# Kernel optimization log

Hardware: AMD Instinct MI355X
Metric: run time of the kernel (lower is better)

The kernel has to match this reference:

```python
import jax, jax.numpy as jnp
import numpy as np
from jax import lax
from jax.scipy.special import logsumexp

C, H, W = 21, 512, 512
ITERS = 5
THETA_GAMMA = 3.0
THETA_ALPHA = 160.0
MAX_RADIUS = 8  # truncation cap for the Gaussian surrogate of the permutohedral filter
# deterministic stand-in for random.sample(range(200,400),1) per iteration
SP_IDS = [250 + 7 * i for i in range(ITERS)]


def _gauss_kernel(sigma):
    radius = min(int(2.0 * sigma + 0.5), MAX_RADIUS)
    t = np.arange(-radius, radius + 1, dtype=np.float32)
    k = np.exp(-0.5 * (t / np.float32(sigma)) ** 2)
    k /= k.sum()
    return jnp.asarray(k)


def _blur(x, k):
    # x: (c,h,w); separable Gaussian blur as surrogate for custom high_dim_filter
    x4 = x[:, None]                      # (c,1,h,w), c acts as batch
    kh = k.reshape(1, 1, -1, 1)
    kw = k.reshape(1, 1, 1, -1)
    y = lax.conv_general_dilated(x4, kh, (1, 1), 'SAME')
    y = lax.conv_general_dilated(y, kw, (1, 1), 'SAME')
    return y[:, 0]


def _sp_containment_update(q, low_w, high_w, sp_map, sp_idx):
    # q: softmax output (c,h,w); sp_map: (h,w) int ids; single clique sp_idx
    cond = (sp_map == sp_idx)                       # (h,w)
    condf = cond.astype(q.dtype)[None]              # (1,h,w) broadcast over c
    q_clique = condf * q                            # masked q
    bool_max = (q == q.max(axis=0, keepdims=True))  # global per-pixel argmax mask
    maxlab = q_clique.max(axis=0, keepdims=True)    # per-pixel max label prob in clique
    l_eq = (bool_max & cond[None]).astype(q.dtype) * q
    A_np = q_clique + maxlab - l_eq                 # "A no padding"
    q_sum = A_np                                    # sum over the single clique
    # per-class logsumexp over the whole plane (zeros outside clique, as in source)
    B_sp = logsumexp(q_clique, axis=(1, 2))         # (c,)
    prod_sp = condf * B_sp[:, None, None]
    B_cont = logsumexp(A_np, axis=(1, 2))           # (c,)
    prod_io = condf * B_cont[:, None, None]         # cond applied twice in source == once
    q_mod = q + (q == 0).astype(q.dtype)
    q_sum = q_sum + (q_sum == 0).astype(q.dtype)
    ft = prod_sp / q_mod
    sp_update = low_w[0][:, None, None] * ft + high_w[0] * (1.0 - ft)
    ft2 = prod_io / q_sum
    cont_update = low_w[1][:, None, None] * ft2 + high_w[1] * (1.0 - ft2)
    return sp_update + cont_update


def setup_inputs() -> dict:
    key = jax.random.key(0)
    k1, k2, k3 = jax.random.split(key, 3)
    unaries = jax.random.normal(k1, (1, H, W, C), dtype=jnp.float32)
    rgb = jax.random.uniform(k2, (1, H, W, 3), dtype=jnp.float32)
    sp_map = jax.random.randint(k3, (1, W, H), 0, 400, dtype=jnp.int32)
    spatial_ker_weights = jnp.eye(C, dtype=jnp.float32)
    bilateral_ker_weights = jnp.eye(C, dtype=jnp.float32)
    complex_rel_low_weights = jnp.ones((2, C), dtype=jnp.float32)
    complex_rel_high_weights = jnp.ones((2,), dtype=jnp.float32)
    compatibility_matrix = -jnp.eye(C, dtype=jnp.float32)
    return {
        'unaries': unaries, 'rgb': rgb, 'sp_map': sp_map,
        'spatial_ker_weights': spatial_ker_weights,
        'bilateral_ker_weights': bilateral_ker_weights,
        'complex_rel_low_weights': complex_rel_low_weights,
        'complex_rel_high_weights': complex_rel_high_weights,
        'compatibility_matrix': compatibility_matrix,
    }


def reference(unaries, rgb, sp_map, spatial_ker_weights, bilateral_ker_weights,
              complex_rel_low_weights, complex_rel_high_weights, compatibility_matrix):
    u = jnp.transpose(unaries[0], (2, 0, 1))   # (c,h,w)
    sp = jnp.transpose(sp_map[0])              # (h,w)
    k_sp = _gauss_kernel(THETA_GAMMA)
    k_bi = _gauss_kernel(THETA_ALPHA)
    ones = jnp.ones((C, H, W), jnp.float32)
    spatial_norm = _blur(ones, k_sp)
    bilateral_norm = _blur(ones, k_bi)
    q = u
    for i in range(ITERS):
        sm = jax.nn.softmax(q, axis=0)
        spatial_out = _blur(sm, k_sp) / spatial_norm
        bilateral_out = _blur(sm, k_bi) / bilateral_norm
        cont = _sp_containment_update(sm, complex_rel_low_weights,
                                      complex_rel_high_weights, sp, SP_IDS[i])
        mp = (jnp.einsum('ij,jhw->ihw', spatial_ker_weights, spatial_out)
              + jnp.einsum('ij,jhw->ihw', bilateral_ker_weights, bilateral_out))
        pairwise = jnp.einsum('ij,jhw->ihw', compatibility_matrix, mp)
        q = u - pairwise - cont
    return jnp.transpose(q, (1, 2, 0))[None]   # (1,h,w,c)
```

## Files before the change

### kernel.cpp

```cpp
#include <hip/hip_runtime.h>
#include <hip/hip_bf16.h>
#include <math.h>
#include <utility>

#define C 21
#define H 512
#define W 512
#define HW (H*W)
#define CHW (C*HW)
#define N_ITERS 5
#define RSP 6
#define KSP 13
#define RBI 8
#define KBI 17
#define LIST_CAP 4096

#define KSP_OFF   0
#define KBI_OFF   16
#define NSP_OFF   64
#define NBI_OFF   576
#define M1_OFF    1088
#define M2_OFF    1536
#define NCOND_OFF 2048
#define S1_OFF    2064
#define S2_OFF    2176
#define CTR_OFF   2288
#define LIST_OFF  2304
#define CONTB_OFF 22784
#define UBH_OFF   131072
#define QB16_OFF  (UBH_OFF + CHW/2)
#define T12_OFF   (QB16_OFF + CHW/2)

#define REP21(F) F(0) F(1) F(2) F(3) F(4) F(5) F(6) F(7) F(8) F(9) F(10) \
                 F(11) F(12) F(13) F(14) F(15) F(16) F(17) F(18) F(19) F(20)

template <int... Js, typename F>
__device__ __forceinline__ void sfor(std::integer_sequence<int, Js...>, F&& f) {
  (f(std::integral_constant<int, Js>{}), ...);
}
#define SFOR(N, ...) sfor(std::make_integer_sequence<int, N>{}, __VA_ARGS__)

__device__ __forceinline__ float bf2f(unsigned short u) {
  return __uint_as_float(((unsigned)u) << 16);
}
__device__ __forceinline__ unsigned short f2bfu(float a) {
  __hip_bfloat16 h = __float2bfloat16(a);
  return *(unsigned short*)&h;
}
__device__ __forceinline__ unsigned packbf(float a, float b) {
  return (unsigned)f2bfu(a) | ((unsigned)f2bfu(b) << 16);
}

__global__ __launch_bounds__(512) void k_setup(float* ws, const float* skw,
                                               const float* bkw, const float* cm) {
  int tid = threadIdx.x;
  if (tid == 0) {
    float s = 0.f;
    for (int i = 0; i < KSP; ++i) {
      float t = (float)(i - RSP);
      float v = expf(-0.5f * (t / 3.0f) * (t / 3.0f));
      ws[KSP_OFF + i] = v; s += v;
    }
    for (int i = 0; i < KSP; ++i) ws[KSP_OFF + i] /= s;
    s = 0.f;
    for (int i = 0; i < KBI; ++i) {
      float t = (float)(i - RBI);
      float v = expf(-0.5f * (t / 160.0f) * (t / 160.0f));
      ws[KBI_OFF + i] = v; s += v;
    }
    for (int i = 0; i < KBI; ++i) ws[KBI_OFF + i] /= s;
  }
  __syncthreads();
  if (tid < H) {
    float nsp = 0.f, nbi = 0.f;
    for (int t = 0; t < KSP; ++t) { int x = tid + t - RSP; if (x >= 0 && x < H) nsp += ws[KSP_OFF + t]; }
    for (int t = 0; t < KBI; ++t) { int x = tid + t - RBI; if (x >= 0 && x < H) nbi += ws[KBI_OFF + t]; }
    ws[NSP_OFF + tid] = 1.f / nsp;
    ws[NBI_OFF + tid] = 1.f / nbi;
  }
  if (tid < C * C) {
    int i = tid / C, j = tid % C;
    float m1 = 0.f, m2 = 0.f;
    for (int k = 0; k < C; ++k) {
      m1 += cm[i * C + k] * skw[k * C + j];
      m2 += cm[i * C + k] * bkw[k * C + j];
    }
    ws[M1_OFF + tid] = m1;
    ws[M2_OFF + tid] = m2;
  }
  if (tid < N_ITERS * C) { ws[S1_OFF + tid] = 0.f; ws[S2_OFF + tid] = 0.f; }
  if (tid < N_ITERS) {
    ((int*)(ws + NCOND_OFF))[tid] = 0;
    ((int*)(ws + CTR_OFF))[tid] = 0;
  }
}

__global__ __launch_bounds__(256) void k_spt_tin(const int* __restrict__ sp_map,
                                                 const float* __restrict__ in,
                                                 int* __restrict__ ncond,
                                                 int* __restrict__ list,
                                                 unsigned* __restrict__ ubh32,
                                                 unsigned* __restrict__ qb32) {
  __shared__ float t[C * 257];
  int tid = threadIdx.x;
  int p = blockIdx.x * 256 + tid;
  {
    int h = p >> 9, w = p & 511;
    int v = sp_map[w * H + h];
#pragma unroll
    for (int i = 0; i < N_ITERS; ++i)
      if (v == 250 + 7 * i) {
        int slot = atomicAdd(&ncond[i], 1);
        if (slot < LIST_CAP) list[i * LIST_CAP + slot] = p;
      }
  }
  size_t p0 = (size_t)blockIdx.x * 256;
  size_t fbase = p0 * C;
#pragma unroll
  for (int i = 0; i < C; ++i) {
    int e = i * 256 + tid;
    int pp = e / C, c = e % C;
    t[c * 257 + pp] = in[fbase + e];
  }
  __syncthreads();
  if (tid < 128) {
#pragma unroll
    for (int c = 0; c < C; ++c) {
      float v0 = t[c * 257 + 2 * tid];
      float v1 = t[c * 257 + 2 * tid + 1];
      unsigned d = packbf(v0, v1);
      size_t di = ((size_t)c * HW + p0) / 2 + tid;
      ubh32[di] = d;
      qb32[di] = d;
    }
  }
}

__global__ __launch_bounds__(256) void k_tout(const unsigned* __restrict__ qb32,
                                              float* __restrict__ out) {
  __shared__ float t[C * 257];
  int tid = threadIdx.x;
  size_t p0 = (size_t)blockIdx.x * 256;
  if (tid < 128) {
#pragma unroll
    for (int c = 0; c < C; ++c) {
      unsigned d = qb32[((size_t)c * HW + p0) / 2 + tid];
      t[c * 257 + 2 * tid] = __uint_as_float(d << 16);
      t[c * 257 + 2 * tid + 1] = __uint_as_float(d & 0xFFFF0000u);
    }
  }
  __syncthreads();
  size_t fbase = p0 * C;
#pragma unroll
  for (int i = 0; i < C; ++i) {
    int e = i * 256 + tid;
    int p = e / C, c = e % C;
    out[fbase + e] = t[c * 257 + p];
  }
}

__global__ __launch_bounds__(256) void k_clique(const unsigned short* __restrict__ qh,
                                                float* __restrict__ ws,
                                                const float* __restrict__ loww,
                                                const float* __restrict__ highw,
                                                int iter) {
  int tid = threadIdx.x;
  const int* ncond = (const int*)(ws + NCOND_OFF);
  const int* list = (const int*)(ws + LIST_OFF) + iter * LIST_CAP;
  int n = ncond[iter]; if (n > LIST_CAP) n = LIST_CAP;
#define D1(i) float s1_##i = 0.f, s2_##i = 0.f;
  REP21(D1)
#undef D1
  for (int j = blockIdx.x * 256 + tid; j < n; j += 1024) {
    int p = list[j];
#define LQ(i) float q##i = __expf(bf2f(qh[(size_t)(i) * HW + p]));
    REP21(LQ)
#undef LQ
    float s = ((((q0+q1)+(q2+q3))+((q4+q5)+(q6+q7)))+(((q8+q9)+(q10+q11))+((q12+q13)+(q14+q15))))+(((q16+q17)+(q18+q19))+q20);
    float inv = 1.f / s;
    float smax = 0.f;
#define NM(i) q##i *= inv; smax = fmaxf(smax, q##i);
    REP21(NM)
#undef NM
#define AC(i) { s1_##i += __expf(q##i); \
                float A = (q##i == smax) ? smax : q##i + smax; \
                s2_##i += __expf(A); }
    REP21(AC)
#undef AC
  }
#define RED(x) x += __shfl_xor(x, 32); x += __shfl_xor(x, 16); x += __shfl_xor(x, 8); \
               x += __shfl_xor(x, 4); x += __shfl_xor(x, 2); x += __shfl_xor(x, 1);
#define RD(i) RED(s1_##i) RED(s2_##i)
  REP21(RD)
#undef RD
#undef RED
  if ((tid & 63) == 0) {
#define AT(i) atomicAdd(&ws[S1_OFF + iter * C + (i)], s1_##i); \
              atomicAdd(&ws[S2_OFF + iter * C + (i)], s2_##i);
    REP21(AT)
#undef AT
  }
  __threadfence();
  __syncthreads();
  if (tid == 0) {
    int* ctr = (int*)(ws + CTR_OFF) + iter;
    atomicAdd(ctr, 1);
    while (atomicAdd(ctr, 0) < 4) { __builtin_amdgcn_s_sleep(1); }
  }
  __syncthreads();
  __threadfence();
  float HWn = (float)(HW - n);
#define LB(i) float lb1_##i = logf(HWn + ws[S1_OFF + iter * C + (i)]); \
              float lb2_##i = logf(HWn + ws[S2_OFF + iter * C + (i)]);
  REP21(LB)
#undef LB
  float high0 = highw[0], high1 = highw[1];
  float* contb = ws + CONTB_OFF;
  for (int j = blockIdx.x * 256 + tid; j < n; j += 1024) {
    int p = list[j];
#define LQ2(i) float q##i = __expf(bf2f(qh[(size_t)(i) * HW + p]));
    REP21(LQ2)
#undef LQ2
    float s = ((((q0+q1)+(q2+q3))+((q4+q5)+(q6+q7)))+(((q8+q9)+(q10+q11))+((q12+q13)+(q14+q15))))+(((q16+q17)+(q18+q19))+q20);
    float inv = 1.f / s;
    float smax = 0.f;
#define NM2(i) q##i *= inv; smax = fmaxf(smax, q##i);
    REP21(NM2)
#undef NM2
#define CW(i) { float A = (q##i == smax) ? smax : q##i + smax; \
                float ft = lb1_##i / q##i; \
                float ft2 = lb2_##i / A; \
                contb[j * C + (i)] = loww[i] * ft + high0 * (1.f - ft) \
                                   + loww[C + (i)] * ft2 + high1 * (1.f - ft2); }
    REP21(CW)
#undef CW
  }
}

__global__ __launch_bounds__(256) void k_smmix(const unsigned* __restrict__ q16x2,
                                               unsigned* __restrict__ t12,
                                               const float* __restrict__ ws) {
  int tid = threadIdx.x;
  int b2 = blockIdx.x * 256 + tid;
#define LQ(i) unsigned d##i = q16x2[(size_t)(i) * (HW/2) + b2]; \
              float ex##i = __expf(__uint_as_float(d##i << 16)); \
              float ey##i = __expf(__uint_as_float(d##i & 0xFFFF0000u));
  REP21(LQ)
#undef LQ
  float sa = ((((ex0+ex1)+(ex2+ex3))+((ex4+ex5)+(ex6+ex7)))+(((ex8+ex9)+(ex10+ex11))+((ex12+ex13)+(ex14+ex15))))+(((ex16+ex17)+(ex18+ex19))+ex20);
  float sb = ((((ey0+ey1)+(ey2+ey3))+((ey4+ey5)+(ey6+ey7)))+(((ey8+ey9)+(ey10+ey11))+((ey12+ey13)+(ey14+ey15))))+(((ey16+ey17)+(ey18+ey19))+ey20);
  float ia = 1.f / sa, ib = 1.f / sb;
#define NQ(i) ex##i *= ia; ey##i *= ib;
  REP21(NQ)
#undef NQ
  for (int i = 0; i < C; ++i) {
    const float* r1 = ws + M1_OFF + i * C;
    const float* r2 = ws + M2_OFF + i * C;
    float t1a = 0.f, t1b = 0.f, t2a = 0.f, t2b = 0.f;
#define MIX(c) { float m1v = r1[c], m2v = r2[c]; \
                 t1a += m1v * ex##c; t1b += m1v * ey##c; \
                 t2a += m2v * ex##c; t2b += m2v * ey##c; }
    REP21(MIX)
#undef MIX
    uint2 st;
    st.x = packbf(t1a, t2a);
    st.y = packbf(t1b, t2b);
    *reinterpret_cast<uint2*>(t12 + (size_t)i * HW + 2 * b2) = st;
  }
}

__global__ __launch_bounds__(256) void k_blur2d(
    const unsigned* __restrict__ t12, const unsigned* __restrict__ uh32,
    unsigned* __restrict__ qout, const float* __restrict__ ws,
    const float* __restrict__ highw) {
  __shared__ float asmem[16 * 152], bsmem[16 * 152];
  __shared__ float ktsp[KSP], ktbi[KBI];
  __shared__ float nspw[128], nbiw[128], nsph[16], nbih[16];
  int tid = threadIdx.x;
  int l = blockIdx.x;
  int nl = (l & 7) * 336 + (l >> 3);
  int c = nl >> 7;
  int rem = nl & 127;
  int h0 = (rem >> 2) * 16;
  int w0 = (rem & 3) * 128;
  if (tid < KSP) ktsp[tid] = ws[KSP_OFF + tid];
  if (tid >= 32 && tid < 32 + KBI) ktbi[tid - 32] = ws[KBI_OFF + tid - 32];
  if (tid >= 64 && tid < 192) {
    int i = tid - 64;
    nspw[i] = ws[NSP_OFF + w0 + i];
    nbiw[i] = ws[NBI_OFF + w0 + i];
  }
  if (tid >= 192 && tid < 208) {
    int i = tid - 192;
    nsph[i] = ws[NSP_OFF + h0 + i];
    nbih[i] = ws[NBI_OFF + h0 + i];
  }
  __syncthreads();
  size_t cbase = (size_t)c * HW;
  if (tid < 144) {
    int col = w0 - 8 + tid;
    bool okc = (col >= 0 && col < W);
    const unsigned* s12 = t12 + cbase;
    unsigned lv[32];
    SFOR(32, [&](auto jc) {
      constexpr int j = decltype(jc)::value;
      int hh = h0 - 8 + j;
      lv[j] = (okc && hh >= 0 && hh < H) ? s12[(size_t)hh * W + col] : 0u;
    });
    float a[16], b[16];
    SFOR(16, [&](auto oc) {
      constexpr int o = decltype(oc)::value;
      a[o] = 0.f; b[o] = 0.f;
    });
    SFOR(32, [&](auto jc) {
      constexpr int j = decltype(jc)::value;
      float f1 = __uint_as_float(lv[j] << 16);
      float f2 = __uint_as_float(lv[j] & 0xFFFF0000u);
      SFOR(16, [&](auto oc) {
        constexpr int o = decltype(oc)::value;
        if constexpr (j - 2 - o >= 0 && j - 2 - o < KSP) a[o] += ktsp[j - 2 - o] * f1;
        if constexpr (j - o >= 0 && j - o < KBI) b[o] += ktbi[j - o] * f2;
      });
    });
    SFOR(16, [&](auto oc) {
      constexpr int o = decltype(oc)::value;
      asmem[o * 152 + tid] = a[o];
      bsmem[o * 152 + tid] = b[o];
    });
  }
  __syncthreads();
  float cc = highw[0] + highw[1];
#pragma unroll
  for (int k = 0; k < 2; ++k) {
    int o = tid + k * 256;
    int r = o >> 5;
    int wq = (o & 31) * 4;
    float aw[16], bw[20];
    const float2* ap = reinterpret_cast<const float2*>(&asmem[r * 152 + wq + 2]);
    const float2* bp = reinterpret_cast<const float2*>(&bsmem[r * 152 + wq]);
    SFOR(8, [&](auto jc) {
      constexpr int j = decltype(jc)::value;
      float2 v = ap[j];
      aw[2 * j] = v.x;
      aw[2 * j + 1] = v.y;
    });
    SFOR(10, [&](auto jc) {
      constexpr int j = decltype(jc)::value;
      float2 v = bp[j];
      bw[2 * j] = v.x;
      bw[2 * j + 1] = v.y;
    });
    float ao[4], bo[4];
    SFOR(4, [&](auto jc) {
      constexpr int j = decltype(jc)::value;
      float s1 = 0.f;
      float s2 = 0.f;
      SFOR(KSP, [&](auto tc) {
        constexpr int t = decltype(tc)::value;
        s1 += ktsp[t] * aw[j + t];
      });
      SFOR(KBI, [&](auto tc) {
        constexpr int t = decltype(tc)::value;
        s2 += ktbi[t] * bw[j + t];
      });
      ao[j] = s1;
      bo[j] = s2;
    });
    int hh = h0 + r, ww = w0 + wq;
    size_t idx = cbase + (size_t)hh * W + ww;
    uint2 uv = *reinterpret_cast<const uint2*>(uh32 + (idx >> 1));
    float u0 = __uint_as_float(uv.x << 16);
    float u1 = __uint_as_float(uv.x & 0xFFFF0000u);
    float u2 = __uint_as_float(uv.y << 16);
    float u3 = __uint_as_float(uv.y & 0xFFFF0000u);
    float nh1 = nsph[r], nh2 = nbih[r];
    float r0 = u0 - (ao[0] * (nh1 * nspw[wq])     + bo[0] * (nh2 * nbiw[wq]))     - cc;
    float r1 = u1 - (ao[1] * (nh1 * nspw[wq + 1]) + bo[1] * (nh2 * nbiw[wq + 1])) - cc;
    float r2 = u2 - (ao[2] * (nh1 * nspw[wq + 2]) + bo[2] * (nh2 * nbiw[wq + 2])) - cc;
    float r3 = u3 - (ao[3] * (nh1 * nspw[wq + 3]) + bo[3] * (nh2 * nbiw[wq + 3])) - cc;
    uint2 st;
    st.x = packbf(r0, r1);
    st.y = packbf(r2, r3);
    *reinterpret_cast<uint2*>(qout + (idx >> 1)) = st;
  }
}

__global__ __launch_bounds__(256) void k_contfix(unsigned short* __restrict__ q16,
                                                 const float* __restrict__ ws,
                                                 const float* __restrict__ highw,
                                                 int iter) {
  const int* ncond = (const int*)(ws + NCOND_OFF);
  int n = ncond[iter]; if (n > LIST_CAP) n = LIST_CAP;
  int e = blockIdx.x * 256 + threadIdx.x;
  if (e >= n * C) return;
  int j = e / C, c = e - j * C;
  const int* list = (const int*)(ws + LIST_OFF) + iter * LIST_CAP;
  int p = list[j];
  float cc = highw[0] + highw[1];
  float delta = cc - ws[CONTB_OFF + e];
  size_t idx = (size_t)c * HW + p;
  q16[idx] = f2bfu(bf2f(q16[idx]) + delta);
}

extern "C" void kernel_launch(void* const* d_in, const int* in_sizes, int n_in,
                              void* d_out, int out_size, void* d_ws, size_t ws_size,
                              hipStream_t stream) {
  const float* unaries = (const float*)d_in[0];
  const int* sp_map = (const int*)d_in[2];
  const float* skw = (const float*)d_in[3];
  const float* bkw = (const float*)d_in[4];
  const float* loww = (const float*)d_in[5];
  const float* highw = (const float*)d_in[6];
  const float* cm = (const float*)d_in[7];
  float* out = (float*)d_out;
  float* ws = (float*)d_ws;
  unsigned* ubh32 = (unsigned*)(ws + UBH_OFF);
  unsigned* qb32 = (unsigned*)(ws + QB16_OFF);
  unsigned short* qh16 = (unsigned short*)(ws + QB16_OFF);
  unsigned* t12 = (unsigned*)(ws + T12_OFF);
  int* ncond = (int*)(ws + NCOND_OFF);
  int* list = (int*)(ws + LIST_OFF);

  k_setup<<<1, 512, 0, stream>>>(ws, skw, bkw, cm);
  k_spt_tin<<<HW / 256, 256, 0, stream>>>(sp_map, unaries, ncond, list, ubh32, qb32);
  for (int i = 0; i < N_ITERS; ++i) {
    k_clique<<<4, 256, 0, stream>>>(qh16, ws, loww, highw, i);
    k_smmix<<<HW / 512, 256, 0, stream>>>(qb32, t12, ws);
    k_blur2d<<<2688, 256, 0, stream>>>(t12, ubh32, qb32, ws, highw);
    k_contfix<<<128, 256, 0, stream>>>(qh16, ws, highw, i);
  }
  k_tout<<<HW / 256, 256, 0, stream>>>(qb32, out);
}
```

Before: 373.2 us.

## Fuse contfix into next clique, drop duplicate q copy, coalesce sp_map reads

Result: slower. 415.6 us (+11.4%).

```diff
diff --git a/kernel.cpp b/kernel.cpp
--- a/kernel.cpp
+++ b/kernel.cpp
@@ -99,14 +99,13 @@
                                                  const float* __restrict__ in,
                                                  int* __restrict__ ncond,
                                                  int* __restrict__ list,
-                                                 unsigned* __restrict__ ubh32,
-                                                 unsigned* __restrict__ qb32) {
+                                                 unsigned* __restrict__ ubh32) {
   __shared__ float t[C * 257];
   int tid = threadIdx.x;
-  int p = blockIdx.x * 256 + tid;
   {
-    int h = p >> 9, w = p & 511;
-    int v = sp_map[w * H + h];
+    int m = blockIdx.x * 256 + tid;
+    int v = sp_map[m];
+    int p = ((m & 511) << 9) | (m >> 9);
 #pragma unroll
     for (int i = 0; i < N_ITERS; ++i)
       if (v == 250 + 7 * i) {
@@ -123,16 +122,11 @@
     t[c * 257 + pp] = in[fbase + e];
   }
   __syncthreads();
-  if (tid < 128) {
-#pragma unroll
-    for (int c = 0; c < C; ++c) {
-      float v0 = t[c * 257 + 2 * tid];
-      float v1 = t[c * 257 + 2 * tid + 1];
-      unsigned d = packbf(v0, v1);
-      size_t di = ((size_t)c * HW + p0) / 2 + tid;
-      ubh32[di] = d;
-      qb32[di] = d;
-    }
+  for (int e = tid; e < C * 128; e += 256) {
+    int c = e >> 7, pr = e & 127;
+    float v0 = t[c * 257 + 2 * pr];
+    float v1 = t[c * 257 + 2 * pr + 1];
+    ubh32[((size_t)c * HW + p0) / 2 + pr] = packbf(v0, v1);
   }
 }
 
@@ -159,7 +153,7 @@
   }
 }
 
-__global__ __launch_bounds__(256) void k_clique(const unsigned short* __restrict__ qh,
+__global__ __launch_bounds__(256) void k_clique(unsigned short* __restrict__ qh,
                                                 float* __restrict__ ws,
                                                 const float* __restrict__ loww,
                                                 const float* __restrict__ highw,
@@ -168,6 +162,18 @@
   const int* ncond = (const int*)(ws + NCOND_OFF);
   const int* list = (const int*)(ws + LIST_OFF) + iter * LIST_CAP;
   int n = ncond[iter]; if (n > LIST_CAP) n = LIST_CAP;
+  float high0 = highw[0], high1 = highw[1];
+  float cc = high0 + high1;
+  if (iter > 0) {
+    int np = ncond[iter - 1]; if (np > LIST_CAP) np = LIST_CAP;
+    const int* plist = (const int*)(ws + LIST_OFF) + (iter - 1) * LIST_CAP;
+    for (int e = blockIdx.x * 256 + tid; e < np * C; e += 1024) {
+      int j = e / C, c = e - j * C;
+      int p = plist[j];
+      size_t idx = (size_t)c * HW + p;
+      qh[idx] = f2bfu(bf2f(qh[idx]) + cc - ws[CONTB_OFF + e]);
+    }
+  }
 #define D1(i) float s1_##i = 0.f, s2_##i = 0.f;
   REP21(D1)
 #undef D1
@@ -214,7 +220,6 @@
               float lb2_##i = logf(HWn + ws[S2_OFF + iter * C + (i)]);
   REP21(LB)
 #undef LB
-  float high0 = highw[0], high1 = highw[1];
   float* contb = ws + CONTB_OFF;
   for (int j = blockIdx.x * 256 + tid; j < n; j += 1024) {
     int p = list[j];
@@ -417,17 +422,20 @@
   unsigned* ubh32 = (unsigned*)(ws + UBH_OFF);
   unsigned* qb32 = (unsigned*)(ws + QB16_OFF);
   unsigned short* qh16 = (unsigned short*)(ws + QB16_OFF);
+  unsigned short* uh16 = (unsigned short*)(ws + UBH_OFF);
   unsigned* t12 = (unsigned*)(ws + T12_OFF);
   int* ncond = (int*)(ws + NCOND_OFF);
   int* list = (int*)(ws + LIST_OFF);
 
   k_setup<<<1, 512, 0, stream>>>(ws, skw, bkw, cm);
-  k_spt_tin<<<HW / 256, 256, 0, stream>>>(sp_map, unaries, ncond, list, ubh32, qb32);
+  k_spt_tin<<<HW / 256, 256, 0, stream>>>(sp_map, unaries, ncond, list, ubh32);
   for (int i = 0; i < N_ITERS; ++i) {
-    k_clique<<<4, 256, 0, stream>>>(qh16, ws, loww, highw, i);
-    k_smmix<<<HW / 512, 256, 0, stream>>>(qb32, t12, ws);
+    unsigned short* qcur16 = (i == 0) ? uh16 : qh16;
+    const unsigned* qcur32 = (i == 0) ? ubh32 : qb32;
+    k_clique<<<4, 256, 0, stream>>>(qcur16, ws, loww, highw, i);
+    k_smmix<<<HW / 512, 256, 0, stream>>>(qcur32, t12, ws);
     k_blur2d<<<2688, 256, 0, stream>>>(t12, ubh32, qb32, ws, highw);
-    k_contfix<<<128, 256, 0, stream>>>(qh16, ws, highw, i);
-  }
+  }
+  k_contfix<<<128, 256, 0, stream>>>(qh16, ws, highw, N_ITERS - 1);
   k_tout<<<HW / 256, 256, 0, stream>>>(qb32, out);
 }
```
